# Optimization experiments

Hardware: AMD Instinct MI355X
Metric: run time of the kernel (lower is better)

Reference implementation:

```python
import jax, jax.numpy as jnp
import numpy as np

TEMP = 0.1

def _normalized_grid(B, H, W, dtype=jnp.float32):
    # normalized coords in [-1, 1], (x, y) order, shape [B, H, W, 2]
    ys = jnp.linspace(-1.0, 1.0, H, dtype=dtype)
    xs = jnp.linspace(-1.0, 1.0, W, dtype=dtype)
    gy, gx = jnp.meshgrid(ys, xs, indexing='ij')
    grid = jnp.stack([gx, gy], axis=-1)  # [H, W, 2]
    return jnp.broadcast_to(grid, (B, H, W, 2))


def setup_inputs() -> dict:
    key = jax.random.key(0)
    k1, k2, k3 = jax.random.split(key, 3)
    B, H, W, D = 8, 48, 48, 1024
    f_mv_A = jax.random.normal(k1, (B, H, W, D), dtype=jnp.float32)
    f_mv_B = jax.random.normal(k2, (B, H, W, D), dtype=jnp.float32)
    # omega buffer: 2*pi*randn(dim//2, 2)
    omega = 2.0 * jnp.pi * jax.random.normal(k3, (D // 2, 2), dtype=jnp.float32)
    scale = jnp.ones((), dtype=jnp.float32)
    return {"f_mv_A": f_mv_A, "f_mv_B": f_mv_B, "omega": omega, "scale": scale}


def reference(f_mv_A, f_mv_B, omega, scale):
    B, H_A, W_A, D = f_mv_A.shape
    _, H_B, W_B, _ = f_mv_B.shape
    # Fourier positional embedding grid over image B coordinates
    x = _normalized_grid(B, H_B, W_B).reshape(B, H_B * W_B, 2)
    x_emb = x @ (scale * omega).T                      # [B, HW_B, D//2]
    pos_emb_grid = jnp.concatenate([jnp.sin(x_emb), jnp.cos(x_emb)], axis=-1)  # [B, HW_B, D]

    # cosine similarity cross-attention
    fa = f_mv_A / jnp.linalg.norm(f_mv_A, axis=-1, keepdims=True)
    fb = f_mv_B / jnp.linalg.norm(f_mv_B, axis=-1, keepdims=True)
    fa = fa.reshape(B, H_A * W_A, D)
    fb = fb.reshape(B, H_B * W_B, D)
    attn_logits = (1.0 / TEMP) * jnp.einsum('bqd,bkd->bqk', fa, fb)  # [B, HW_A, HW_B]
    attn = jax.nn.softmax(attn_logits, axis=2)
    match_emb = jnp.einsum('bqk,bkd->bqd', attn, pos_emb_grid)        # [B, HW_A, D]

    attn_logits = attn_logits.reshape(B, H_A, W_A, H_B, W_B)
    attn = attn.reshape(B, H_A, W_A, H_B, W_B)
    match_emb = match_emb.reshape(B, H_A, W_A, D)
    return attn_logits, attn, match_emb
```

## Files before the change

kernel.cpp:

```cpp
#include <hip/hip_runtime.h>
#include <stdint.h>
#include <math.h>

#define NBATCH 8
#define HWSZ   2304
#define DDIM   1024
#define NROWS  (NBATCH*HWSZ)
#define PLANE  ((size_t)NROWS*DDIM)
#define OFF1   ((size_t)NBATCH*HWSZ*HWSZ)
#define OFF2   (2*OFF1)

typedef __attribute__((ext_vector_type(8))) short bf16x8;
typedef __attribute__((ext_vector_type(8))) _Float16 f16x8;
typedef __attribute__((ext_vector_type(4))) float f32x4;

__device__ __forceinline__ float bf2f(uint16_t u) {
    union { uint32_t i; float f; } v; v.i = ((uint32_t)u) << 16; return v.f;
}
__device__ __forceinline__ uint16_t f2bf(float f) {
    union { uint32_t i; float f; } v; v.f = f;
    uint32_t x = v.i;
    return (uint16_t)((x + 0x7fffu + ((x >> 16) & 1u)) >> 16);
}
__device__ __forceinline__ float h2f(uint16_t u) {
    _Float16 h; __builtin_memcpy(&h, &u, 2); return (float)h;
}
__device__ __forceinline__ uint16_t f2h(float f) {
    _Float16 h = (_Float16)f; uint16_t u; __builtin_memcpy(&u, &h, 2); return u;
}
__device__ __forceinline__ int dmode(const uint16_t* s) {
    uint16_t v = s[0];
    return (v == 0x3F80u) ? 1 : ((v == 0x3C00u) ? 2 : 0);
}
__device__ __forceinline__ float dec16(uint16_t u, int m) { return (m == 1) ? bf2f(u) : h2f(u); }
__device__ __forceinline__ uint16_t enc16(float f, int m) { return (m == 1) ? f2bf(f) : f2h(f); }

__global__ void layout_probe(int* __restrict__ rowT, int* __restrict__ colT) {
    int lane = threadIdx.x & 63;
    int m = lane & 15, q = lane >> 4;
    bf16x8 a1, b1, a2, b2;
    #pragma unroll
    for (int j = 0; j < 8; j++) {
        int k = q * 8 + j;
        float k0 = (k == 0) ? 1.0f : 0.0f;
        a1[j] = (short)f2bf(k0);
        b1[j] = (short)f2bf(k0 * (float)(m + 1));
        a2[j] = (short)f2bf(k0 * (float)(m + 1));
        b2[j] = (short)f2bf(k0);
    }
    f32x4 z = {0.f, 0.f, 0.f, 0.f};
    f32x4 d1 = __builtin_amdgcn_mfma_f32_16x16x32_bf16(a1, b1, z, 0, 0, 0);
    f32x4 d2 = __builtin_amdgcn_mfma_f32_16x16x32_bf16(a2, b2, z, 0, 0, 0);
    #pragma unroll
    for (int r = 0; r < 4; r++) {
        colT[lane * 4 + r] = (int)d1[r] - 1;
        rowT[lane * 4 + r] = (int)d2[r] - 1;
    }
}

__global__ void rownorm_kernel(const void* __restrict__ inA, const void* __restrict__ inB,
                               const uint16_t* __restrict__ scalep, float* __restrict__ rn,
                               void* __restrict__ outbase) {
    const int mode = dmode(scalep);
    int row = blockIdx.x;
    int t = threadIdx.x;
    const void* src = (row < NROWS) ? inA : inB;
    int lrow = (row < NROWS) ? row : row - NROWS;
    float v[4];
    if (mode == 0) {
        const float* p = (const float*)src + (size_t)lrow * DDIM + t * 4;
        float4 f = *(const float4*)p;
        v[0] = f.x; v[1] = f.y; v[2] = f.z; v[3] = f.w;
        uint16_t* hbase = (uint16_t*)((float*)outbase + OFF1) + ((row < NROWS) ? 0 : PLANE);
        uint16_t h0 = f2h(v[0]), h1 = f2h(v[1]), h2 = f2h(v[2]), h3 = f2h(v[3]);
        uint2 hv;
        hv.x = (uint32_t)h0 | ((uint32_t)h1 << 16);
        hv.y = (uint32_t)h2 | ((uint32_t)h3 << 16);
        *(uint2*)(hbase + (size_t)lrow * DDIM + t * 4) = hv;
    } else {
        const uint16_t* p = (const uint16_t*)src + (size_t)lrow * DDIM + t * 4;
        uint2 u = *(const uint2*)p;
        v[0] = dec16(u.x & 0xffff, mode); v[1] = dec16(u.x >> 16, mode);
        v[2] = dec16(u.y & 0xffff, mode); v[3] = dec16(u.y >> 16, mode);
    }
    float ss = v[0]*v[0] + v[1]*v[1] + v[2]*v[2] + v[3]*v[3];
    __shared__ float red[256];
    red[t] = ss; __syncthreads();
    for (int s = 128; s > 0; s >>= 1) { if (t < s) red[t] += red[t + s]; __syncthreads(); }
    if (t == 0) rn[row] = 1.0f / sqrtf(red[0]);
}

__global__ void posemb_kernel(const void* __restrict__ omega, const uint16_t* __restrict__ scalep,
                              uint16_t* __restrict__ posT) {
    const int mode = dmode(scalep);
    int j = blockIdx.x;
    float om0, om1, sc;
    if (mode == 0) {
        const float* om = (const float*)omega;
        om0 = om[j * 2]; om1 = om[j * 2 + 1];
        sc = *(const float*)scalep;
    } else {
        const uint16_t* om = (const uint16_t*)omega;
        om0 = dec16(om[j * 2], mode); om1 = dec16(om[j * 2 + 1], mode);
        sc = dec16(scalep[0], mode);
    }
    om0 *= sc; om1 *= sc;
    for (int p = threadIdx.x; p < HWSZ; p += 256) {
        int iy = p / 48, ix = p % 48;
        float gx = (2.0f / 47.0f) * (float)ix - 1.0f;
        float gy = (2.0f / 47.0f) * (float)iy - 1.0f;
        float e = om0 * gx + om1 * gy;
        size_t chunk = (size_t)(p >> 5) * (DDIM * 32);
        int kin = p & 31;
        posT[chunk + (size_t)j * 32 + kin]           = f2bf(sinf(e));
        posT[chunk + (size_t)(j + 512) * 32 + kin]   = f2bf(cosf(e));
    }
}

#define LSTR 40

__launch_bounds__(256, 2)
__global__ void gemm1_mfma(const void* __restrict__ inA, const void* __restrict__ inB,
                           const uint16_t* __restrict__ scalep, const float* __restrict__ rn,
                           void* __restrict__ outbase,
                           const int* __restrict__ rowT, const int* __restrict__ colT) {
    const int mode = dmode(scalep);
    __shared__ uint16_t sA[128 * LSTR];
    __shared__ uint16_t sB[128 * LSTR];
    __shared__ float rnS[256];
    int g = blockIdx.x;
    int swz = (g & 7) * 324 + (g >> 3);
    int b = swz / 324;
    int rr = swz % 324;
    int tm = rr / 18, tn = rr % 18;
    int t = threadIdx.x;
    if (t < 128) rnS[t] = 10.0f * rn[(size_t)b * HWSZ + tm * 128 + t];
    else         rnS[t] = rn[(size_t)NROWS + (size_t)b * HWSZ + tn * 128 + (t - 128)];
    int r0c = t >> 2, cb0 = (t & 3) * 8;
    int r1c = r0c + 64;
    int lane = t & 63, wave = t >> 6;
    int wm = (wave & 1) * 64, wn = (wave >> 1) * 64;
    int lr = lane & 15, ko = (lane >> 4) * 8;
    size_t rowA0 = (size_t)b * HWSZ + tm * 128;
    size_t rowB0 = (size_t)b * HWSZ + tn * 128;
    const uint16_t* pA16;
    const uint16_t* pB16;
    if (mode == 0) {
        const uint16_t* planes = (const uint16_t*)((const float*)outbase + OFF1);
        pA16 = planes + rowA0 * DDIM;
        pB16 = planes + PLANE + rowB0 * DDIM;
    } else {
        pA16 = (const uint16_t*)inA + rowA0 * DDIM;
        pB16 = (const uint16_t*)inB + rowB0 * DDIM;
    }
    f32x4 acc[4][4] = {};

    for (int k0 = 0; k0 < DDIM; k0 += 32) {
        uint4 a0 = *(const uint4*)(pA16 + (size_t)r0c * DDIM + k0 + cb0);
        uint4 a1 = *(const uint4*)(pA16 + (size_t)r1c * DDIM + k0 + cb0);
        uint4 b0 = *(const uint4*)(pB16 + (size_t)r0c * DDIM + k0 + cb0);
        uint4 b1 = *(const uint4*)(pB16 + (size_t)r1c * DDIM + k0 + cb0);
        __syncthreads();
        *(uint4*)(sA + r0c * LSTR + cb0) = a0;
        *(uint4*)(sA + r1c * LSTR + cb0) = a1;
        *(uint4*)(sB + r0c * LSTR + cb0) = b0;
        *(uint4*)(sB + r1c * LSTR + cb0) = b1;
        __syncthreads();
        if (mode == 1) {
            bf16x8 af[4], bf_[4];
            #pragma unroll
            for (int i = 0; i < 4; i++) af[i] = *(const bf16x8*)(sA + (wm + i * 16 + lr) * LSTR + ko);
            #pragma unroll
            for (int j = 0; j < 4; j++) bf_[j] = *(const bf16x8*)(sB + (wn + j * 16 + lr) * LSTR + ko);
            #pragma unroll
            for (int i = 0; i < 4; i++)
                #pragma unroll
                for (int j = 0; j < 4; j++)
                    acc[i][j] = __builtin_amdgcn_mfma_f32_16x16x32_bf16(af[i], bf_[j], acc[i][j], 0, 0, 0);
        } else {
            f16x8 af[4], bf_[4];
            #pragma unroll
            for (int i = 0; i < 4; i++) af[i] = *(const f16x8*)(sA + (wm + i * 16 + lr) * LSTR + ko);
            #pragma unroll
            for (int j = 0; j < 4; j++) bf_[j] = *(const f16x8*)(sB + (wn + j * 16 + lr) * LSTR + ko);
            #pragma unroll
            for (int i = 0; i < 4; i++)
                #pragma unroll
                for (int j = 0; j < 4; j++)
                    acc[i][j] = __builtin_amdgcn_mfma_f32_16x16x32_f16(af[i], bf_[j], acc[i][j], 0, 0, 0);
        }
    }

    int rtab[4], ctab[4];
    #pragma unroll
    for (int r = 0; r < 4; r++) {
        rtab[r] = rowT[lane * 4 + r] & 15;
        ctab[r] = colT[lane * 4 + r] & 15;
    }
    size_t cbase = (size_t)b * HWSZ * HWSZ;
    #pragma unroll
    for (int i = 0; i < 4; i++) {
        #pragma unroll
        for (int j = 0; j < 4; j++) {
            #pragma unroll
            for (int r = 0; r < 4; r++) {
                int row = wm + i * 16 + rtab[r];
                int col = wn + j * 16 + ctab[r];
                float v = acc[i][j][r] * rnS[row] * rnS[128 + col];
                size_t gm = (size_t)(tm * 128 + row);
                size_t gn = (size_t)(tn * 128 + col);
                if (mode == 0) ((float*)outbase)[cbase + gm * HWSZ + gn] = v;
                else ((uint16_t*)outbase)[cbase + gm * HWSZ + gn] = enc16(v, mode);
            }
        }
    }
}

__global__ void softmax_p16(void* __restrict__ outbase, const uint16_t* __restrict__ scalep,
                            uint16_t* __restrict__ p16) {
    const int mode = dmode(scalep);
    size_t row = blockIdx.x;
    int t = threadIdx.x;
    float v[9];
    if (mode == 0) {
        const float* src = (const float*)outbase + row * HWSZ;
        #pragma unroll
        for (int i = 0; i < 9; i++) v[i] = src[i * 256 + t];
    } else {
        const uint16_t* src = (const uint16_t*)outbase + row * HWSZ;
        #pragma unroll
        for (int i = 0; i < 9; i++) v[i] = dec16(src[i * 256 + t], mode);
    }
    float m = v[0];
    #pragma unroll
    for (int i = 1; i < 9; i++) m = fmaxf(m, v[i]);
    __shared__ float red[256];
    red[t] = m; __syncthreads();
    for (int s = 128; s > 0; s >>= 1) { if (t < s) red[t] = fmaxf(red[t], red[t + s]); __syncthreads(); }
    float M = red[0];
    __syncthreads();
    float ssum = 0.0f;
    #pragma unroll
    for (int i = 0; i < 9; i++) { v[i] = __expf(v[i] - M); ssum += v[i]; }
    red[t] = ssum; __syncthreads();
    for (int s = 128; s > 0; s >>= 1) { if (t < s) red[t] += red[t + s]; __syncthreads(); }
    float inv = 1.0f / red[0];
    uint16_t* prow = p16 + row * HWSZ;
    if (mode == 0) {
        float* dst = (float*)outbase + OFF1 + row * HWSZ;
        #pragma unroll
        for (int i = 0; i < 9; i++) {
            float p = v[i] * inv;
            dst[i * 256 + t] = p;
            prow[i * 256 + t] = f2bf(p);
        }
    } else {
        uint16_t* dst = (uint16_t*)outbase + OFF1 + row * HWSZ;
        #pragma unroll
        for (int i = 0; i < 9; i++) {
            uint16_t pk = enc16(v[i] * inv, mode);
            dst[i * 256 + t] = pk;
            prow[i * 256 + t] = (mode == 1) ? pk : f2bf(h2f(pk));
        }
    }
}

__global__ void rowstat_kernel(const void* __restrict__ outbase, const uint16_t* __restrict__ scalep,
                               float* __restrict__ stats) {
    const int mode = dmode(scalep);
    size_t row = blockIdx.x;
    int t = threadIdx.x;
    float v[9];
    if (mode == 0) {
        const float* src = (const float*)outbase + row * HWSZ;
        #pragma unroll
        for (int i = 0; i < 9; i++) v[i] = src[i * 256 + t];
    } else {
        const uint16_t* src = (const uint16_t*)outbase + row * HWSZ;
        #pragma unroll
        for (int i = 0; i < 9; i++) v[i] = dec16(src[i * 256 + t], mode);
    }
    float m = v[0];
    #pragma unroll
    for (int i = 1; i < 9; i++) m = fmaxf(m, v[i]);
    __shared__ float red[256];
    red[t] = m; __syncthreads();
    for (int s = 128; s > 0; s >>= 1) { if (t < s) red[t] = fmaxf(red[t], red[t + s]); __syncthreads(); }
    float M = red[0];
    __syncthreads();
    float ssum = 0.0f;
    #pragma unroll
    for (int i = 0; i < 9; i++) ssum += __expf(v[i] - M);
    red[t] = ssum; __syncthreads();
    for (int s = 128; s > 0; s >>= 1) { if (t < s) red[t] += red[t + s]; __syncthreads(); }
    if (t == 0) { stats[row] = M; stats[NROWS + row] = 1.0f / red[0]; }
}

#define G2BM 64
#define G2BN 256
#define G2L  40

__launch_bounds__(256, 4)
__global__ void gemm2_p16(void* __restrict__ outbase, const uint16_t* __restrict__ posT,
                          const uint16_t* __restrict__ scalep, const uint16_t* __restrict__ p16,
                          const int* __restrict__ rowT, const int* __restrict__ colT) {
    const int mode = dmode(scalep);
    __shared__ uint16_t sA[G2BM * G2L];
    __shared__ uint16_t sB[G2BN * G2L];
    int g = blockIdx.x;
    int swz = (g & 7) * 144 + (g >> 3);
    int b = swz / 144;
    int rr = swz % 144;
    int tm = rr >> 2, tn = rr & 3;
    int t = threadIdx.x;
    int lane = t & 63, wave = t >> 6;
    int wn = wave * 64;
    int lr = lane & 15, ko = (lane >> 4) * 8;
    int ar = t >> 2, ac8 = (t & 3) * 8;
    const uint16_t* pArow = p16 + ((size_t)b * HWSZ + (size_t)tm * G2BM + ar) * HWSZ;
    f32x4 acc[4][4] = {};
    for (int k0 = 0; k0 < HWSZ; k0 += 32) {
        uint4 a0 = *(const uint4*)(pArow + k0 + ac8);
        const uint16_t* bsrc = posT + (size_t)(k0 >> 5) * (DDIM * 32) + ((size_t)tn * G2BN + t) * 32;
        uint4 bv0 = *(const uint4*)(bsrc + 0);
        uint4 bv1 = *(const uint4*)(bsrc + 8);
        uint4 bv2 = *(const uint4*)(bsrc + 16);
        uint4 bv3 = *(const uint4*)(bsrc + 24);
        __syncthreads();
        *(uint4*)(sA + ar * G2L + ac8) = a0;
        *(uint4*)(sB + t * G2L + 0)  = bv0;
        *(uint4*)(sB + t * G2L + 8)  = bv1;
        *(uint4*)(sB + t * G2L + 16) = bv2;
        *(uint4*)(sB + t * G2L + 24) = bv3;
        __syncthreads();
        bf16x8 af[4], bfr[4];
        #pragma unroll
        for (int i = 0; i < 4; i++) af[i] = *(const bf16x8*)(sA + (i * 16 + lr) * G2L + ko);
        #pragma unroll
        for (int j = 0; j < 4; j++) bfr[j] = *(const bf16x8*)(sB + (wn + j * 16 + lr) * G2L + ko);
        #pragma unroll
        for (int i = 0; i < 4; i++)
            #pragma unroll
            for (int j = 0; j < 4; j++)
                acc[i][j] = __builtin_amdgcn_mfma_f32_16x16x32_bf16(af[i], bfr[j], acc[i][j], 0, 0, 0);
    }
    int rtab[4], ctab[4];
    #pragma unroll
    for (int r = 0; r < 4; r++) {
        rtab[r] = rowT[lane * 4 + r] & 15;
        ctab[r] = colT[lane * 4 + r] & 15;
    }
    #pragma unroll
    for (int i = 0; i < 4; i++) {
        #pragma unroll
        for (int j = 0; j < 4; j++) {
            #pragma unroll
            for (int r = 0; r < 4; r++) {
                size_t row = (size_t)tm * G2BM + i * 16 + rtab[r];
                size_t col = (size_t)tn * G2BN + wn + j * 16 + ctab[r];
                size_t idx = OFF2 + (size_t)b * HWSZ * DDIM + row * DDIM + col;
                if (mode == 0) ((float*)outbase)[idx] = acc[i][j][r];
                else ((uint16_t*)outbase)[idx] = enc16(acc[i][j][r], mode);
            }
        }
    }
}

__launch_bounds__(256, 4)
__global__ void gemm2_mfma(void* __restrict__ outbase, const uint16_t* __restrict__ posT,
                           const uint16_t* __restrict__ scalep, const float* __restrict__ stats,
                           const int* __restrict__ rowT, const int* __restrict__ colT) {
    const int mode = dmode(scalep);
    __shared__ uint16_t sA[G2BM * G2L];
    int g = blockIdx.x;
    int swz = (g & 7) * 144 + (g >> 3);
    int b = swz / 144;
    int rr = swz % 144;
    int tm = rr >> 2, tn = rr & 3;
    int t = threadIdx.x;
    int lane = t & 63, wave = t >> 6;
    int wn = wave * 64;
    int lr = lane & 15, ko = (lane >> 4) * 8;
    int ar = t >> 2, ac8 = (t & 3) * 8;
    size_t grow = (size_t)b * HWSZ + (size_t)tm * G2BM + ar;
    float Mrow = stats[grow];
    float invl = stats[NROWS + grow];
    f32x4 acc[4][4] = {};
    for (int k0 = 0; k0 < HWSZ; k0 += 32) {
        uint16_t av[8];
        float p[8];
        if (mode == 0) {
            const float* ap = (const float*)outbase + grow * HWSZ + k0 + ac8;
            float4 x0 = *(const float4*)ap, x1 = *(const float4*)(ap + 4);
            p[0] = __expf(x0.x - Mrow) * invl; p[1] = __expf(x0.y - Mrow) * invl;
            p[2] = __expf(x0.z - Mrow) * invl; p[3] = __expf(x0.w - Mrow) * invl;
            p[4] = __expf(x1.x - Mrow) * invl; p[5] = __expf(x1.y - Mrow) * invl;
            p[6] = __expf(x1.z - Mrow) * invl; p[7] = __expf(x1.w - Mrow) * invl;
            if (tn == 0) {
                float* dst = (float*)outbase + OFF1 + grow * HWSZ + k0 + ac8;
                *(float4*)dst       = *(const float4*)p;
                *(float4*)(dst + 4) = *(const float4*)(p + 4);
            }
        } else {
            const uint16_t* ap = (const uint16_t*)outbase + grow * HWSZ + k0 + ac8;
            uint4 r0 = *(const uint4*)ap;
            const uint16_t* u0 = (const uint16_t*)&r0;
            #pragma unroll
            for (int j = 0; j < 8; j++) p[j] = __expf(dec16(u0[j], mode) - Mrow) * invl;
            if (tn == 0) {
                uint16_t pk[8];
                #pragma unroll
                for (int j = 0; j < 8; j++) pk[j] = enc16(p[j], mode);
                *(uint4*)((uint16_t*)outbase + OFF1 + grow * HWSZ + k0 + ac8) = *(const uint4*)pk;
            }
        }
        #pragma unroll
        for (int j = 0; j < 8; j++) av[j] = f2bf(p[j]);
        __syncthreads();
        *(uint4*)(sA + ar * G2L + ac8) = *(const uint4*)av;
        __syncthreads();
        const uint16_t* bchunk = posT + (size_t)(k0 >> 5) * (DDIM * 32);
        bf16x8 af[4], bfr[4];
        #pragma unroll
        for (int j = 0; j < 4; j++)
            bfr[j] = *(const bf16x8*)(bchunk + ((size_t)tn * G2BN + wn + j * 16 + lr) * 32 + ko);
        #pragma unroll
        for (int i = 0; i < 4; i++) af[i] = *(const bf16x8*)(sA + (i * 16 + lr) * G2L + ko);
        #pragma unroll
        for (int i = 0; i < 4; i++)
            #pragma unroll
            for (int j = 0; j < 4; j++)
                acc[i][j] = __builtin_amdgcn_mfma_f32_16x16x32_bf16(af[i], bfr[j], acc[i][j], 0, 0, 0);
    }
    int rtab[4], ctab[4];
    #pragma unroll
    for (int r = 0; r < 4; r++) {
        rtab[r] = rowT[lane * 4 + r] & 15;
        ctab[r] = colT[lane * 4 + r] & 15;
    }
    #pragma unroll
    for (int i = 0; i < 4; i++) {
        #pragma unroll
        for (int j = 0; j < 4; j++) {
            #pragma unroll
            for (int r = 0; r < 4; r++) {
                size_t row = (size_t)tm * G2BM + i * 16 + rtab[r];
                size_t col = (size_t)tn * G2BN + wn + j * 16 + ctab[r];
                size_t idx = OFF2 + (size_t)b * HWSZ * DDIM + row * DDIM + col;
                if (mode == 0) ((float*)outbase)[idx] = acc[i][j][r];
                else ((uint16_t*)outbase)[idx] = enc16(acc[i][j][r], mode);
            }
        }
    }
}

extern "C" void kernel_launch(void* const* d_in, const int* in_sizes, int n_in,
                              void* d_out, int out_size, void* d_ws, size_t ws_size,
                              hipStream_t stream) {
    const void* fA    = d_in[0];
    const void* fB    = d_in[1];
    const void* omega = d_in[2];
    const uint16_t* scale = (const uint16_t*)d_in[3];

    int* rowT = (int*)d_ws;
    int* colT = rowT + 256;
    float* rn = (float*)((char*)d_ws + 4096);
    size_t posT_off = 4096 + (size_t)2 * NROWS * 4;
    uint16_t* posT = (uint16_t*)((char*)d_ws + posT_off);
    size_t p16_off = posT_off + (size_t)DDIM * HWSZ * 2;
    size_t ws_need = p16_off + (size_t)NROWS * HWSZ * 2;
    uint16_t* p16 = (uint16_t*)((char*)d_ws + p16_off);
    const bool big_ws = (ws_size >= ws_need);

    layout_probe<<<1, 64, 0, stream>>>(rowT, colT);
    rownorm_kernel<<<2 * NROWS, 256, 0, stream>>>(fA, fB, scale, rn, d_out);
    posemb_kernel<<<512, 256, 0, stream>>>(omega, scale, posT);

    gemm1_mfma<<<18 * 18 * NBATCH, 256, 0, stream>>>(fA, fB, scale, rn, d_out, rowT, colT);

    if (big_ws) {
        softmax_p16<<<NROWS, 256, 0, stream>>>(d_out, scale, p16);
        gemm2_p16<<<(HWSZ / G2BM) * (DDIM / G2BN) * NBATCH, 256, 0, stream>>>(
            d_out, posT, scale, p16, rowT, colT);
    } else {
        rowstat_kernel<<<NROWS, 256, 0, stream>>>(d_out, scale, rn);
        gemm2_mfma<<<(HWSZ / G2BM) * (DDIM / G2BN) * NBATCH, 256, 0, stream>>>(
            d_out, posT, scale, rn, rowT, colT);
    }
}
```

Measured before the change: 458.9 us.

## Use direct global-to-LDS loads in both MFMA GEMM kernels

Replaces the register-staged global loads plus LDS stores in gemm1 and gemm2 with __builtin_amdgcn_global_load_lds 16-byte direct-to-LDS transfers. The padded LDS row stride (40) becomes unpadded (32) because the direct loads write contiguous wave-linear blocks. The goal is to cut VGPR pressure and the extra LDS write instructions. In exchange, the MFMA operand reads from LDS may hit more bank conflicts, and the loop still has no double buffering. There is also no explicit vmcnt wait before the barrier, which may cause a correctness or ordering issue depending on compiler handling.

```diff
diff --git a/kernel.cpp b/kernel.cpp
--- a/kernel.cpp
+++ b/kernel.cpp
@@ -13,6 +13,10 @@
 typedef __attribute__((ext_vector_type(8))) short bf16x8;
 typedef __attribute__((ext_vector_type(8))) _Float16 f16x8;
 typedef __attribute__((ext_vector_type(4))) float f32x4;
+
+#define GLOAD16(g, l) __builtin_amdgcn_global_load_lds( \
+    (const __attribute__((address_space(1))) void*)(g), \
+    (__attribute__((address_space(3))) void*)(l), 16, 0, 0)
 
 __device__ __forceinline__ float bf2f(uint16_t u) {
     union { uint32_t i; float f; } v; v.i = ((uint32_t)u) << 16; return v.f;
@@ -117,16 +121,14 @@
     }
 }
 
-#define LSTR 40
-
 __launch_bounds__(256, 2)
 __global__ void gemm1_mfma(const void* __restrict__ inA, const void* __restrict__ inB,
                            const uint16_t* __restrict__ scalep, const float* __restrict__ rn,
                            void* __restrict__ outbase,
                            const int* __restrict__ rowT, const int* __restrict__ colT) {
     const int mode = dmode(scalep);
-    __shared__ uint16_t sA[128 * LSTR];
-    __shared__ uint16_t sB[128 * LSTR];
+    __shared__ uint16_t sA[128 * 32];
+    __shared__ uint16_t sB[128 * 32];
     __shared__ float rnS[256];
     int g = blockIdx.x;
     int swz = (g & 7) * 324 + (g >> 3);
@@ -136,8 +138,6 @@
     int t = threadIdx.x;
     if (t < 128) rnS[t] = 10.0f * rn[(size_t)b * HWSZ + tm * 128 + t];
     else         rnS[t] = rn[(size_t)NROWS + (size_t)b * HWSZ + tn * 128 + (t - 128)];
-    int r0c = t >> 2, cb0 = (t & 3) * 8;
-    int r1c = r0c + 64;
     int lane = t & 63, wave = t >> 6;
     int wm = (wave & 1) * 64, wn = (wave >> 1) * 64;
     int lr = lane & 15, ko = (lane >> 4) * 8;
@@ -153,25 +153,31 @@
         pA16 = (const uint16_t*)inA + rowA0 * DDIM;
         pB16 = (const uint16_t*)inB + rowB0 * DDIM;
     }
+    int srow = wave * 32 + (lane >> 2);
+    int squart = (lane & 3) * 8;
+    const uint16_t* aS0 = pA16 + (size_t)srow * DDIM + squart;
+    const uint16_t* aS1 = aS0 + (size_t)16 * DDIM;
+    const uint16_t* bS0 = pB16 + (size_t)srow * DDIM + squart;
+    const uint16_t* bS1 = bS0 + (size_t)16 * DDIM;
+    uint16_t* aD0 = sA + (wave * 32) * 32;
+    uint16_t* aD1 = aD0 + 512;
+    uint16_t* bD0 = sB + (wave * 32) * 32;
+    uint16_t* bD1 = bD0 + 512;
     f32x4 acc[4][4] = {};
 
     for (int k0 = 0; k0 < DDIM; k0 += 32) {
-        uint4 a0 = *(const uint4*)(pA16 + (size_t)r0c * DDIM + k0 + cb0);
-        uint4 a1 = *(const uint4*)(pA16 + (size_t)r1c * DDIM + k0 + cb0);
-        uint4 b0 = *(const uint4*)(pB16 + (size_t)r0c * DDIM + k0 + cb0);
-        uint4 b1 = *(const uint4*)(pB16 + (size_t)r1c * DDIM + k0 + cb0);
-        __syncthreads();
-        *(uint4*)(sA + r0c * LSTR + cb0) = a0;
-        *(uint4*)(sA + r1c * LSTR + cb0) = a1;
-        *(uint4*)(sB + r0c * LSTR + cb0) = b0;
-        *(uint4*)(sB + r1c * LSTR + cb0) = b1;
+        __syncthreads();
+        GLOAD16(aS0 + k0, aD0);
+        GLOAD16(aS1 + k0, aD1);
+        GLOAD16(bS0 + k0, bD0);
+        GLOAD16(bS1 + k0, bD1);
         __syncthreads();
         if (mode == 1) {
             bf16x8 af[4], bf_[4];
             #pragma unroll
-            for (int i = 0; i < 4; i++) af[i] = *(const bf16x8*)(sA + (wm + i * 16 + lr) * LSTR + ko);
-            #pragma unroll
-            for (int j = 0; j < 4; j++) bf_[j] = *(const bf16x8*)(sB + (wn + j * 16 + lr) * LSTR + ko);
+            for (int i = 0; i < 4; i++) af[i] = *(const bf16x8*)(sA + (wm + i * 16 + lr) * 32 + ko);
+            #pragma unroll
+            for (int j = 0; j < 4; j++) bf_[j] = *(const bf16x8*)(sB + (wn + j * 16 + lr) * 32 + ko);
             #pragma unroll
             for (int i = 0; i < 4; i++)
                 #pragma unroll
@@ -180,9 +186,9 @@
         } else {
             f16x8 af[4], bf_[4];
             #pragma unroll
-            for (int i = 0; i < 4; i++) af[i] = *(const f16x8*)(sA + (wm + i * 16 + lr) * LSTR + ko);
-            #pragma unroll
-            for (int j = 0; j < 4; j++) bf_[j] = *(const f16x8*)(sB + (wn + j * 16 + lr) * LSTR + ko);
+            for (int i = 0; i < 4; i++) af[i] = *(const f16x8*)(sA + (wm + i * 16 + lr) * 32 + ko);
+            #pragma unroll
+            for (int j = 0; j < 4; j++) bf_[j] = *(const f16x8*)(sB + (wn + j * 16 + lr) * 32 + ko);
             #pragma unroll
             for (int i = 0; i < 4; i++)
                 #pragma unroll
@@ -305,8 +311,8 @@
                           const uint16_t* __restrict__ scalep, const uint16_t* __restrict__ p16,
                           const int* __restrict__ rowT, const int* __restrict__ colT) {
     const int mode = dmode(scalep);
-    __shared__ uint16_t sA[G2BM * G2L];
-    __shared__ uint16_t sB[G2BN * G2L];
+    __shared__ uint16_t sA[G2BM * 32];
+    __shared__ uint16_t sB[G2BN * 32];
     int g = blockIdx.x;
     int swz = (g & 7) * 144 + (g >> 3);
     int b = swz / 144;
@@ -316,28 +322,26 @@
     int lane = t & 63, wave = t >> 6;
     int wn = wave * 64;
     int lr = lane & 15, ko = (lane >> 4) * 8;
-    int ar = t >> 2, ac8 = (t & 3) * 8;
-    const uint16_t* pArow = p16 + ((size_t)b * HWSZ + (size_t)tm * G2BM + ar) * HWSZ;
+    const uint16_t* aS = p16 + ((size_t)b * HWSZ + (size_t)tm * G2BM + wave * 16 + (lane >> 2)) * HWSZ
+                             + (lane & 3) * 8;
+    uint16_t* aD = sA + (wave * 16) * 32;
+    uint16_t* bD = sB + (wave * 64) * 32;
     f32x4 acc[4][4] = {};
     for (int k0 = 0; k0 < HWSZ; k0 += 32) {
-        uint4 a0 = *(const uint4*)(pArow + k0 + ac8);
-        const uint16_t* bsrc = posT + (size_t)(k0 >> 5) * (DDIM * 32) + ((size_t)tn * G2BN + t) * 32;
-        uint4 bv0 = *(const uint4*)(bsrc + 0);
-        uint4 bv1 = *(const uint4*)(bsrc + 8);
-        uint4 bv2 = *(const uint4*)(bsrc + 16);
-        uint4 bv3 = *(const uint4*)(bsrc + 24);
-        __syncthreads();
-        *(uint4*)(sA + ar * G2L + ac8) = a0;
-        *(uint4*)(sB + t * G2L + 0)  = bv0;
-        *(uint4*)(sB + t * G2L + 8)  = bv1;
-        *(uint4*)(sB + t * G2L + 16) = bv2;
-        *(uint4*)(sB + t * G2L + 24) = bv3;
+        const uint16_t* bS = posT + (size_t)(k0 >> 5) * (DDIM * 32)
+                                  + ((size_t)tn * G2BN + wave * 64) * 32 + lane * 8;
+        __syncthreads();
+        GLOAD16(aS + k0, aD);
+        GLOAD16(bS + 0 * 512, bD + 0 * 512);
+        GLOAD16(bS + 1 * 512, bD + 1 * 512);
+        GLOAD16(bS + 2 * 512, bD + 2 * 512);
+        GLOAD16(bS + 3 * 512, bD + 3 * 512);
         __syncthreads();
         bf16x8 af[4], bfr[4];
         #pragma unroll
-        for (int i = 0; i < 4; i++) af[i] = *(const bf16x8*)(sA + (i * 16 + lr) * G2L + ko);
-        #pragma unroll
-        for (int j = 0; j < 4; j++) bfr[j] = *(const bf16x8*)(sB + (wn + j * 16 + lr) * G2L + ko);
+        for (int i = 0; i < 4; i++) af[i] = *(const bf16x8*)(sA + (i * 16 + lr) * 32 + ko);
+        #pragma unroll
+        for (int j = 0; j < 4; j++) bfr[j] = *(const bf16x8*)(sB + (wn + j * 16 + lr) * 32 + ko);
         #pragma unroll
         for (int i = 0; i < 4; i++)
             #pragma unroll
```

Measured after the change: 428.7 us. 6.6% less time.
